# Optimization experiments

Measured on AMD Instinct MI355X. Metric: run time of the kernel, lower is better.

Reference implementation:

```python
import jax, jax.numpy as jnp
import numpy as np

N_NODES = 50000
N_EDGES = 600000
IN_CH = 128
HID_CH = 128
OUT_CH = 16
N_GRAPHS = 512


def gcn_conv(x, edge_index, W, b, n_nodes):
    """PyG GCNConv: add self-loops, symmetric deg normalization, linear, scatter-add."""
    src = edge_index[0]
    dst = edge_index[1]
    loop = jnp.arange(n_nodes, dtype=edge_index.dtype)
    src = jnp.concatenate([src, loop])  # [E+N]
    dst = jnp.concatenate([dst, loop])
    ones = jnp.ones(src.shape[0], dtype=x.dtype)
    deg = jax.ops.segment_sum(ones, dst, num_segments=n_nodes)  # in-degree incl. self-loop
    dinv = jnp.where(deg > 0, jax.lax.rsqrt(deg), 0.0)
    norm = dinv[src] * dinv[dst]  # [E+N]
    h = x @ W  # [N, out] linear-then-propagate, as in PyG GCNConv
    msg = h[src] * norm[:, None]  # gather + scale
    out = jax.ops.segment_sum(msg, dst, num_segments=n_nodes)
    return out + b


def global_mean_pool(x, batch, num_graphs):
    sums = jax.ops.segment_sum(x, batch, num_segments=num_graphs)
    cnt = jax.ops.segment_sum(jnp.ones(x.shape[0], dtype=x.dtype), batch, num_segments=num_graphs)
    return sums / jnp.maximum(cnt, 1.0)[:, None]


def setup_inputs() -> dict:
    key = jax.random.key(0)
    ks = jax.random.split(key, 8)
    x = jax.random.normal(ks[0], (N_NODES, IN_CH), dtype=jnp.float32)
    edge_index = jax.random.randint(ks[1], (2, N_EDGES), 0, N_NODES, dtype=jnp.int64 if jax.config.jax_enable_x64 else jnp.int32)
    batch = jnp.sort(jax.random.randint(ks[2], (N_NODES,), 0, N_GRAPHS, dtype=edge_index.dtype))
    s1 = 1.0 / np.sqrt(IN_CH)
    s2 = 1.0 / np.sqrt(HID_CH)
    W1 = jax.random.uniform(ks[3], (IN_CH, HID_CH), jnp.float32, -s1, s1)
    b1 = jnp.zeros((HID_CH,), jnp.float32)
    W2 = jax.random.uniform(ks[4], (HID_CH, HID_CH), jnp.float32, -s2, s2)
    b2 = jnp.zeros((HID_CH,), jnp.float32)
    Wfc = jax.random.uniform(ks[5], (HID_CH, OUT_CH), jnp.float32, -s2, s2)
    bfc = jax.random.uniform(ks[6], (OUT_CH,), jnp.float32, -s2, s2)
    return {"x": x, "edge_index": edge_index, "batch": batch,
            "W1": W1, "b1": b1, "W2": W2, "b2": b2, "Wfc": Wfc, "bfc": bfc}


def reference(x, edge_index, batch, W1, b1, W2, b2, Wfc, bfc):
    n = x.shape[0]
    h = jax.nn.relu(gcn_conv(x, edge_index, W1, b1, n))
    # dropout is identity in eval mode (training=False)
    h = jax.nn.relu(gcn_conv(h, edge_index, W2, b2, n))
    g = global_mean_pool(h, batch, N_GRAPHS)  # [G, hidden]
    out = jax.nn.sigmoid(g @ Wfc + bfc)  # [G, out]
    return out
```

## Files before the change

kernel.cpp:

```cpp
#include <hip/hip_runtime.h>
#include <hip/hip_fp16.h>
#include <math.h>

#define NN 50000
#define CH 128
#define NG 512
#define OCH 16
#define CAP 64
#define NBINS 196
#define HB 147

typedef _Float16 half8 __attribute__((ext_vector_type(8)));
typedef float f32x4 __attribute__((ext_vector_type(4)));
typedef float f32x2 __attribute__((ext_vector_type(2)));


__device__ __forceinline__ void unpack_fp8x8(unsigned a0, unsigned a1, float* o) {
    f32x2 a = __builtin_amdgcn_cvt_pk_f32_fp8((int)a0, false);
    f32x2 b = __builtin_amdgcn_cvt_pk_f32_fp8((int)a0, true);
    f32x2 c = __builtin_amdgcn_cvt_pk_f32_fp8((int)a1, false);
    f32x2 d = __builtin_amdgcn_cvt_pk_f32_fp8((int)a1, true);
    o[0] = a[0]; o[1] = a[1]; o[2] = b[0]; o[3] = b[1];
    o[4] = c[0]; o[5] = c[1]; o[6] = d[0]; o[7] = d[1];
}

__device__ __forceinline__ void unpack_fp8x16(uint4 v, float* o) {
    unpack_fp8x8(v.x, v.y, o);
    unpack_fp8x8(v.z, v.w, o + 8);
}

__device__ __forceinline__ unsigned char f32_to_fp8(float v) {
    int r = __builtin_amdgcn_cvt_pk_fp8_f32(v, v, 0, false);
    return (unsigned char)(r & 0xFF);
}


__device__ __forceinline__ void gemm1_body(const float* __restrict__ A, const _Float16* __restrict__ Wt,
                                           unsigned char* __restrict__ C, int n, int blk) {
    int wave = threadIdx.x >> 6;
    int lane = threadIdx.x & 63;
    int base = blk * 64 + wave * 16;
    if (base >= n) return;
    int ma = lane & 15;
    int kb = lane >> 4;

    f32x4 acc[8];
#pragma unroll
    for (int t = 0; t < 8; ++t) acc[t] = (f32x4){0.f, 0.f, 0.f, 0.f};

#pragma unroll
    for (int kk = 0; kk < 4; ++kk) {
        int k0 = kk * 32 + kb * 8;
        const float* ap = A + (size_t)(base + ma) * CH + k0;
        float4 a0 = ((const float4*)ap)[0];
        float4 a1 = ((const float4*)ap)[1];
        half8 af;
        af[0] = (_Float16)a0.x; af[1] = (_Float16)a0.y; af[2] = (_Float16)a0.z; af[3] = (_Float16)a0.w;
        af[4] = (_Float16)a1.x; af[5] = (_Float16)a1.y; af[6] = (_Float16)a1.z; af[7] = (_Float16)a1.w;
#pragma unroll
        for (int tn = 0; tn < 8; ++tn) {
            half8 bf = *(const half8*)(Wt + (size_t)(tn * 16 + ma) * CH + k0);
            acc[tn] = __builtin_amdgcn_mfma_f32_16x16x32_f16(af, bf, acc[tn], 0, 0, 0);
        }
    }

    int r0 = base + kb * 4;
#pragma unroll
    for (int tn = 0; tn < 8; ++tn) {
#pragma unroll
        for (int r = 0; r < 4; ++r) {
            C[(size_t)(r0 + r) * CH + tn * 16 + ma] = f32_to_fp8(acc[tn][r]);
        }
    }
}


__global__ __launch_bounds__(256) void k1_hist_init_gemm1_k(const int* __restrict__ dst, int e, int* __restrict__ tableT,
                                                            const int* __restrict__ batch, int n, int* __restrict__ gstart,
                                                            const float* __restrict__ W1, const float* __restrict__ W2,
                                                            _Float16* __restrict__ Wt1, _Float16* __restrict__ Wt2,
                                                            const float* __restrict__ x, unsigned char* __restrict__ h1,
                                                            int* __restrict__ tickets) {
    if ((int)blockIdx.x < HB) {
        __shared__ int hist[NBINS];
        for (int i = threadIdx.x; i < NBINS; i += 256) hist[i] = 0;
        __syncthreads();
#pragma unroll
        for (int j = 0; j < 4; ++j) {
            int idx = blockIdx.x * 4096 + j * 1024 + threadIdx.x * 4;
            if (idx + 3 < e) {
                int4 d = *(const int4*)&dst[idx];
                atomicAdd(&hist[d.x >> 8], 1);
                atomicAdd(&hist[d.y >> 8], 1);
                atomicAdd(&hist[d.z >> 8], 1);
                atomicAdd(&hist[d.w >> 8], 1);
            } else {
                for (int k = idx; k < e && k < idx + 4; ++k) atomicAdd(&hist[dst[k] >> 8], 1);
            }
        }
        __syncthreads();
        for (int i = threadIdx.x; i < NBINS; i += 256) tableT[i * HB + blockIdx.x] = hist[i];
    } else if ((int)blockIdx.x < HB + 66) {
        int i = ((int)blockIdx.x - HB) * 256 + threadIdx.x;
        if (i < 2) tickets[i] = 0;
        if (i <= NG) {
            int lo = 0, hi = n;
            while (lo < hi) {
                int mid = (lo + hi) >> 1;
                if (batch[mid] < i) lo = mid + 1; else hi = mid;
            }
            gstart[i] = lo;
        }
        if (i < CH * CH) {
            int k = i >> 7, c = i & 127;
            Wt1[c * CH + k] = (_Float16)W1[i];
            Wt2[c * CH + k] = (_Float16)W2[i];
        }
    } else {
        gemm1_body(x, Wt1, h1, n, blockIdx.x - (HB + 66));
    }
}


__global__ __launch_bounds__(256) void scanAB_k(int* __restrict__ tableT, int* __restrict__ binsum,
                                                int* __restrict__ bin_start, int* __restrict__ ticket) {
    int w = threadIdx.x >> 6, lane = threadIdx.x & 63;
    int bin = blockIdx.x * 4 + w;
    {
        int* row = tableT + bin * HB;
        int b3 = lane * 3;
        int v0 = (b3     < HB) ? row[b3]     : 0;
        int v1 = (b3 + 1 < HB) ? row[b3 + 1] : 0;
        int v2 = (b3 + 2 < HB) ? row[b3 + 2] : 0;
        int s = v0 + v1 + v2;
        int x = s;
#pragma unroll
        for (int off = 1; off < 64; off <<= 1) {
            int y = __shfl_up(x, off);
            if (lane >= off) x += y;
        }
        int excl = x - s;
        if (b3     < HB) row[b3]     = excl;
        if (b3 + 1 < HB) row[b3 + 1] = excl + v0;
        if (b3 + 2 < HB) row[b3 + 2] = excl + v0 + v1;
        if (lane == 63) binsum[bin] = x;
    }
    __syncthreads();
    __threadfence();
    __shared__ int lastBlk;
    if (threadIdx.x == 0) lastBlk = (atomicAdd(ticket, 1) == (int)gridDim.x - 1) ? 1 : 0;
    __syncthreads();
    if (lastBlk) {
        __threadfence();
        __shared__ int s[256];
        int t = threadIdx.x;
        int v = (t < NBINS) ? binsum[t] : 0;
        s[t] = v;
        __syncthreads();
        for (int off = 1; off < 256; off <<= 1) {
            int u = (t >= off) ? s[t - off] : 0;
            __syncthreads();
            s[t] += u;
            __syncthreads();
        }
        if (t < NBINS) bin_start[t] = s[t] - v;
        if (t == NBINS - 1) bin_start[NBINS] = s[t];
    }
}


__global__ __launch_bounds__(256) void scatter_k(const int* __restrict__ src, const int* __restrict__ dst, int e,
                                                 const int* __restrict__ tableT, const int* __restrict__ bin_start,
                                                 unsigned int* __restrict__ binned) {
    __shared__ int cur[NBINS];
    for (int i = threadIdx.x; i < NBINS; i += 256) cur[i] = bin_start[i] + tableT[i * HB + blockIdx.x];
    __syncthreads();
#pragma unroll
    for (int j = 0; j < 4; ++j) {
        int idx = blockIdx.x * 4096 + j * 1024 + threadIdx.x * 4;
        if (idx + 3 < e) {
            int4 d = *(const int4*)&dst[idx];
            int4 s = *(const int4*)&src[idx];
            int p0 = atomicAdd(&cur[d.x >> 8], 1);
            int p1 = atomicAdd(&cur[d.y >> 8], 1);
            int p2 = atomicAdd(&cur[d.z >> 8], 1);
            int p3 = atomicAdd(&cur[d.w >> 8], 1);
            binned[p0] = (unsigned)s.x | ((unsigned)(d.x & 255) << 16);
            binned[p1] = (unsigned)s.y | ((unsigned)(d.y & 255) << 16);
            binned[p2] = (unsigned)s.z | ((unsigned)(d.z & 255) << 16);
            binned[p3] = (unsigned)s.w | ((unsigned)(d.w & 255) << 16);
        } else {
            for (int k = idx; k < e && k < idx + 4; ++k) {
                int d = dst[k];
                int p = atomicAdd(&cur[d >> 8], 1);
                binned[p] = (unsigned)src[k] | ((unsigned)(d & 255) << 16);
            }
        }
    }
}


__global__ __launch_bounds__(256) void bucket_k(const unsigned int* __restrict__ binned,
                                                const int* __restrict__ bin_start,
                                                int* __restrict__ cursor, int* __restrict__ csr, int n) {
    __shared__ int cur2[256];
    cur2[threadIdx.x] = 0;
    __syncthreads();
    int lo = bin_start[blockIdx.x], hi = bin_start[blockIdx.x + 1];
    for (int i = lo + threadIdx.x; i < hi; i += 256) {
        unsigned int p = binned[i];
        int local = p >> 16;
        int node = ((int)blockIdx.x << 8) | local;
        int pos = atomicAdd(&cur2[local], 1);
        if (pos < CAP) csr[(size_t)node * CAP + pos] = (int)(p & 0xFFFFu);
    }
    __syncthreads();
    int node = blockIdx.x * 256 + threadIdx.x;
    if (node < n) cursor[node] = cur2[threadIdx.x];
}


__global__ __launch_bounds__(256) void agg1_gemm2_k(const unsigned char* __restrict__ h1,
                                                    const int* __restrict__ cursor, const int* __restrict__ csr,
                                                    const float* __restrict__ b1, const _Float16* __restrict__ Wt2,
                                                    unsigned char* __restrict__ h2, int n) {
    __shared__ _Float16 xs[32][136];
    int local = threadIdx.x >> 3;
    int node = blockIdx.x * 32 + local;
    int lane = threadIdx.x & 7;
    const uint4* H = (const uint4*)h1;

    if (node < n) {
        int deg = cursor[node];
        float dv = rsqrtf((float)deg + 1.0f);
        int degc = deg > CAP ? CAP : deg;

        float acc[16];
        {
            float t[16];
            unpack_fp8x16(H[(size_t)node * 8 + lane], t);
#pragma unroll
            for (int j = 0; j < 16; ++j) acc[j] = t[j] * dv;
        }
        const int4* row4 = (const int4*)(csr + (size_t)node * CAP);
        int i = 0;
        for (; i + 4 <= degc; i += 4) {
            int4 s4 = row4[i >> 2];
            uint4 v0 = H[(size_t)s4.x * 8 + lane];
            uint4 v1 = H[(size_t)s4.y * 8 + lane];
            uint4 v2 = H[(size_t)s4.z * 8 + lane];
            uint4 v3 = H[(size_t)s4.w * 8 + lane];
            float w0 = rsqrtf((float)cursor[s4.x] + 1.0f);
            float w1 = rsqrtf((float)cursor[s4.y] + 1.0f);
            float w2 = rsqrtf((float)cursor[s4.z] + 1.0f);
            float w3 = rsqrtf((float)cursor[s4.w] + 1.0f);
            float t0[16], t1[16], t2[16], t3[16];
            unpack_fp8x16(v0, t0); unpack_fp8x16(v1, t1);
            unpack_fp8x16(v2, t2); unpack_fp8x16(v3, t3);
#pragma unroll
            for (int j = 0; j < 16; ++j) {
                acc[j] = fmaf(t0[j], w0, acc[j]);
                acc[j] = fmaf(t1[j], w1, acc[j]);
                acc[j] = fmaf(t2[j], w2, acc[j]);
                acc[j] = fmaf(t3[j], w3, acc[j]);
            }
        }
        for (; i < degc; ++i) {
            int s = csr[(size_t)node * CAP + i];
            float w = rsqrtf((float)cursor[s] + 1.0f);
            float t[16];
            unpack_fp8x16(H[(size_t)s * 8 + lane], t);
#pragma unroll
            for (int j = 0; j < 16; ++j) acc[j] = fmaf(t[j], w, acc[j]);
        }

        half8 hv0, hv1;
#pragma unroll
        for (int q = 0; q < 4; ++q) {
            float4 bb = ((const float4*)b1)[4 * lane + q];
            float r0 = fmaxf(fmaf(acc[4 * q + 0], dv, bb.x), 0.f);
            float r1 = fmaxf(fmaf(acc[4 * q + 1], dv, bb.y), 0.f);
            float r2 = fmaxf(fmaf(acc[4 * q + 2], dv, bb.z), 0.f);
            float r3 = fmaxf(fmaf(acc[4 * q + 3], dv, bb.w), 0.f);
            if (q < 2) {
                hv0[4 * q + 0] = (_Float16)r0; hv0[4 * q + 1] = (_Float16)r1;
                hv0[4 * q + 2] = (_Float16)r2; hv0[4 * q + 3] = (_Float16)r3;
            } else {
                hv1[4 * (q - 2) + 0] = (_Float16)r0; hv1[4 * (q - 2) + 1] = (_Float16)r1;
                hv1[4 * (q - 2) + 2] = (_Float16)r2; hv1[4 * (q - 2) + 3] = (_Float16)r3;
            }
        }
        ((half8*)&xs[local][lane * 16])[0] = hv0;
        ((half8*)&xs[local][lane * 16])[1] = hv1;
    } else {
        half8 z = (half8){0, 0, 0, 0, 0, 0, 0, 0};
        ((half8*)&xs[local][lane * 16])[0] = z;
        ((half8*)&xs[local][lane * 16])[1] = z;
    }
    __syncthreads();

    int wave = threadIdx.x >> 6;
    int l = threadIdx.x & 63;
    int ma = l & 15;
    int kb = l >> 4;
    f32x4 acc00 = (f32x4){0.f, 0.f, 0.f, 0.f}, acc01 = acc00, acc10 = acc00, acc11 = acc00;
#pragma unroll
    for (int kk = 0; kk < 4; ++kk) {
        int k0 = kk * 32 + kb * 8;
        half8 af0 = *(const half8*)&xs[ma][k0];
        half8 af1 = *(const half8*)&xs[16 + ma][k0];
        half8 bf0 = *(const half8*)(Wt2 + (size_t)((wave * 2 + 0) * 16 + ma) * CH + k0);
        half8 bf1 = *(const half8*)(Wt2 + (size_t)((wave * 2 + 1) * 16 + ma) * CH + k0);
        acc00 = __builtin_amdgcn_mfma_f32_16x16x32_f16(af0, bf0, acc00, 0, 0, 0);
        acc01 = __builtin_amdgcn_mfma_f32_16x16x32_f16(af0, bf1, acc01, 0, 0, 0);
        acc10 = __builtin_amdgcn_mfma_f32_16x16x32_f16(af1, bf0, acc10, 0, 0, 0);
        acc11 = __builtin_amdgcn_mfma_f32_16x16x32_f16(af1, bf1, acc11, 0, 0, 0);
    }
    int base = blockIdx.x * 32;
#pragma unroll
    for (int rt = 0; rt < 2; ++rt) {
        int gr0 = base + rt * 16 + kb * 4;
        float dv2[4];
#pragma unroll
        for (int r = 0; r < 4; ++r) dv2[r] = (gr0 + r < n) ? rsqrtf((float)cursor[gr0 + r] + 1.0f) : 0.f;
#pragma unroll
        for (int ct = 0; ct < 2; ++ct) {
            int tn = wave * 2 + ct;
            f32x4 a = (rt == 0) ? (ct == 0 ? acc00 : acc01) : (ct == 0 ? acc10 : acc11);
#pragma unroll
            for (int r = 0; r < 4; ++r) {
                if (gr0 + r < n)
                    h2[(size_t)(gr0 + r) * CH + tn * 16 + ma] = f32_to_fp8(a[r] * dv2[r]);
            }
        }
    }
}


__global__ __launch_bounds__(1024) void agg2_pool_fc_k(const unsigned char* __restrict__ h2,
                                                       const int* __restrict__ cursor, const int* __restrict__ csr,
                                                       const float* __restrict__ b2, const int* __restrict__ gstart,
                                                       const float* __restrict__ Wfc, const float* __restrict__ bfc,
                                                       float* __restrict__ out) {
    __shared__ float psum[128][128];
    __shared__ float psum2[8][128];
    int g = blockIdx.x;
    int group = threadIdx.x >> 3;
    int lane = threadIdx.x & 7;
    int beg = gstart[g], end = gstart[g + 1];
    int c = end - beg;
    const uint4* H = (const uint4*)h2;

    float bias[16];
#pragma unroll
    for (int q = 0; q < 4; ++q) {
        float4 bb = ((const float4*)b2)[4 * lane + q];
        bias[4 * q + 0] = bb.x; bias[4 * q + 1] = bb.y;
        bias[4 * q + 2] = bb.z; bias[4 * q + 3] = bb.w;
    }

    float racc[16];
#pragma unroll
    for (int j = 0; j < 16; ++j) racc[j] = 0.f;

    for (int node = beg + group; node < end; node += 128) {
        int deg = cursor[node];
        float dv = rsqrtf((float)deg + 1.0f);
        int degc = deg > CAP ? CAP : deg;

        float acc[16];
        unpack_fp8x16(H[(size_t)node * 8 + lane], acc);

        const int4* row4 = (const int4*)(csr + (size_t)node * CAP);
        int i = 0;
        for (; i + 4 <= degc; i += 4) {
            int4 s4 = row4[i >> 2];
            uint4 v0 = H[(size_t)s4.x * 8 + lane];
            uint4 v1 = H[(size_t)s4.y * 8 + lane];
            uint4 v2 = H[(size_t)s4.z * 8 + lane];
            uint4 v3 = H[(size_t)s4.w * 8 + lane];
            float t0[16], t1[16], t2[16], t3[16];
            unpack_fp8x16(v0, t0); unpack_fp8x16(v1, t1);
            unpack_fp8x16(v2, t2); unpack_fp8x16(v3, t3);
#pragma unroll
            for (int j = 0; j < 16; ++j) acc[j] += (t0[j] + t1[j]) + (t2[j] + t3[j]);
        }
        for (; i < degc; ++i) {
            int s = csr[(size_t)node * CAP + i];
            float t[16];
            unpack_fp8x16(H[(size_t)s * 8 + lane], t);
#pragma unroll
            for (int j = 0; j < 16; ++j) acc[j] += t[j];
        }

#pragma unroll
        for (int j = 0; j < 16; ++j) racc[j] += fmaxf(fmaf(acc[j], dv, bias[j]), 0.f);
    }

#pragma unroll
    for (int q = 0; q < 4; ++q) {
        float4 v;
        v.x = racc[4 * q + 0]; v.y = racc[4 * q + 1];
        v.z = racc[4 * q + 2]; v.w = racc[4 * q + 3];
        ((float4*)&psum[group][lane * 16])[q] = v;
    }
    __syncthreads();

    {
        int ch = threadIdx.x & 127;
        int seg = threadIdx.x >> 7;
        float s = 0.f;
#pragma unroll
        for (int gg = seg * 16; gg < seg * 16 + 16; ++gg) s += psum[gg][ch];
        psum2[seg][ch] = s;
    }
    __syncthreads();
    int t = threadIdx.x;
    if (t < CH) {
        float s = 0.f;
#pragma unroll
        for (int ss = 0; ss < 8; ++ss) s += psum2[ss][t];
        psum2[0][t] = s / fmaxf((float)c, 1.0f);
    }
    __syncthreads();
    if (t < OCH) {
        float acc = bfc[t];
#pragma unroll 8
        for (int k = 0; k < CH; ++k) acc = fmaf(psum2[0][k], Wfc[k * OCH + t], acc);
        out[(size_t)g * OCH + t] = 1.0f / (1.0f + expf(-acc));
    }
}

extern "C" void kernel_launch(void* const* d_in, const int* in_sizes, int n_in,
                              void* d_out, int out_size, void* d_ws, size_t ws_size,
                              hipStream_t stream) {
    const float* x    = (const float*)d_in[0];
    const int*   edge = (const int*)d_in[1];
    const int*   batch= (const int*)d_in[2];
    const float* W1   = (const float*)d_in[3];
    const float* b1   = (const float*)d_in[4];
    const float* W2   = (const float*)d_in[5];
    const float* b2   = (const float*)d_in[6];
    const float* Wfc  = (const float*)d_in[7];
    const float* bfc  = (const float*)d_in[8];
    float* out = (float*)d_out;

    const int N = NN;
    const int E = in_sizes[1] / 2;
    const int* src = edge;
    const int* dst = edge + E;

    unsigned char* h1 = (unsigned char*)d_ws;
    unsigned char* h2 = h1 + (size_t)N * CH;
    _Float16* Wt1     = (_Float16*)(h2 + (size_t)N * CH);
    _Float16* Wt2     = Wt1 + CH * CH;
    int* cursor       = (int*)(Wt2 + CH * CH);
    int* gstart       = cursor + N;
    int* csr          = gstart + NG + 4;
    int* tableT       = csr + (size_t)N * CAP;
    int* binsum       = tableT + NBINS * HB;
    int* bin_start    = binsum + 256;
    int* tickets      = bin_start + 208;
    unsigned int* binned = (unsigned int*)(tickets + 16);

    const int G = (N + 63) / 64;

    k1_hist_init_gemm1_k<<<HB + 66 + G, 256, 0, stream>>>(dst, E, tableT, batch, N, gstart,
                                                          W1, W2, Wt1, Wt2, x, h1, tickets);
    scanAB_k<<<49, 256, 0, stream>>>(tableT, binsum, bin_start, &tickets[0]);
    scatter_k<<<HB, 256, 0, stream>>>(src, dst, E, tableT, bin_start, binned);
    bucket_k<<<NBINS, 256, 0, stream>>>(binned, bin_start, cursor, csr, N);
    agg1_gemm2_k<<<(N + 31) / 32, 256, 0, stream>>>(h1, cursor, csr, b1, Wt2, h2, N);
    agg2_pool_fc_k<<<NG, 1024, 0, stream>>>(h2, cursor, csr, b2, gstart, Wfc, bfc, out);
}
```

Before: 105.5 us.

## Split layer-2 features into channel halves and precompute fp16 inverse sqrt degrees

The layer-2 hidden features are now stored as two 64-channel halves, and the final aggregation/pool kernel runs twice, once per half. Each pass gathers a smaller working set, which should fit better in cache. The second pass combines both halves for the FC layer. Per-node inverse sqrt degrees are also computed once in the bucketing kernel as fp16, so the layer-1 aggregation loads a 2-byte weight instead of reading the int degree and calling rsqrt per edge. The costs are an extra kernel launch, re-reading the CSR lists twice, and reduced precision in the normalization weights.

New measurement: 103.4 us. 1.02x faster.

```diff
diff --git a/kernel.cpp b/kernel.cpp
--- a/kernel.cpp
+++ b/kernel.cpp
@@ -202,7 +202,8 @@
 
 __global__ __launch_bounds__(256) void bucket_k(const unsigned int* __restrict__ binned,
                                                 const int* __restrict__ bin_start,
-                                                int* __restrict__ cursor, int* __restrict__ csr, int n) {
+                                                int* __restrict__ cursor, int* __restrict__ csr,
+                                                __half* __restrict__ dinv16, int n) {
     __shared__ int cur2[256];
     cur2[threadIdx.x] = 0;
     __syncthreads();
@@ -216,14 +217,20 @@
     }
     __syncthreads();
     int node = blockIdx.x * 256 + threadIdx.x;
-    if (node < n) cursor[node] = cur2[threadIdx.x];
+    if (node < n) {
+        int deg = cur2[threadIdx.x];
+        cursor[node] = deg;
+        dinv16[node] = __float2half(rsqrtf((float)deg + 1.0f));
+    }
 }
 
 
 __global__ __launch_bounds__(256) void agg1_gemm2_k(const unsigned char* __restrict__ h1,
                                                     const int* __restrict__ cursor, const int* __restrict__ csr,
+                                                    const __half* __restrict__ dinv16,
                                                     const float* __restrict__ b1, const _Float16* __restrict__ Wt2,
-                                                    unsigned char* __restrict__ h2, int n) {
+                                                    unsigned char* __restrict__ h2a, unsigned char* __restrict__ h2b,
+                                                    int n) {
     __shared__ _Float16 xs[32][136];
     int local = threadIdx.x >> 3;
     int node = blockIdx.x * 32 + local;
@@ -250,10 +257,10 @@
             uint4 v1 = H[(size_t)s4.y * 8 + lane];
             uint4 v2 = H[(size_t)s4.z * 8 + lane];
             uint4 v3 = H[(size_t)s4.w * 8 + lane];
-            float w0 = rsqrtf((float)cursor[s4.x] + 1.0f);
-            float w1 = rsqrtf((float)cursor[s4.y] + 1.0f);
-            float w2 = rsqrtf((float)cursor[s4.z] + 1.0f);
-            float w3 = rsqrtf((float)cursor[s4.w] + 1.0f);
+            float w0 = __half2float(dinv16[s4.x]);
+            float w1 = __half2float(dinv16[s4.y]);
+            float w2 = __half2float(dinv16[s4.z]);
+            float w3 = __half2float(dinv16[s4.w]);
             float t0[16], t1[16], t2[16], t3[16];
             unpack_fp8x16(v0, t0); unpack_fp8x16(v1, t1);
             unpack_fp8x16(v2, t2); unpack_fp8x16(v3, t3);
@@ -267,7 +274,7 @@
         }
         for (; i < degc; ++i) {
             int s = csr[(size_t)node * CAP + i];
-            float w = rsqrtf((float)cursor[s] + 1.0f);
+            float w = __half2float(dinv16[s]);
             float t[16];
             unpack_fp8x16(H[(size_t)s * 8 + lane], t);
 #pragma unroll
@@ -326,35 +333,40 @@
 #pragma unroll
         for (int ct = 0; ct < 2; ++ct) {
             int tn = wave * 2 + ct;
+            int col = tn * 16 + ma;
+            unsigned char* dstp = (col < 64) ? h2a : h2b;
+            int cidx = col & 63;
             f32x4 a = (rt == 0) ? (ct == 0 ? acc00 : acc01) : (ct == 0 ? acc10 : acc11);
 #pragma unroll
             for (int r = 0; r < 4; ++r) {
                 if (gr0 + r < n)
-                    h2[(size_t)(gr0 + r) * CH + tn * 16 + ma] = f32_to_fp8(a[r] * dv2[r]);
-            }
-        }
-    }
-}
-
-
-__global__ __launch_bounds__(1024) void agg2_pool_fc_k(const unsigned char* __restrict__ h2,
-                                                       const int* __restrict__ cursor, const int* __restrict__ csr,
-                                                       const float* __restrict__ b2, const int* __restrict__ gstart,
-                                                       const float* __restrict__ Wfc, const float* __restrict__ bfc,
-                                                       float* __restrict__ out) {
-    __shared__ float psum[128][128];
-    __shared__ float psum2[8][128];
+                    dstp[(size_t)(gr0 + r) * 64 + cidx] = f32_to_fp8(a[r] * dv2[r]);
+            }
+        }
+    }
+}
+
+
+template <int HALF>
+__global__ __launch_bounds__(512) void agg2_half_k(const unsigned char* __restrict__ h2h,
+                                                   const int* __restrict__ cursor, const int* __restrict__ csr,
+                                                   const float* __restrict__ b2, const int* __restrict__ gstart,
+                                                   float* __restrict__ pooled0,
+                                                   const float* __restrict__ Wfc, const float* __restrict__ bfc,
+                                                   float* __restrict__ out) {
+    __shared__ float psum[128][64];
+    __shared__ float psum2[8][64];
     int g = blockIdx.x;
-    int group = threadIdx.x >> 3;
-    int lane = threadIdx.x & 7;
+    int group = threadIdx.x >> 2;
+    int lane = threadIdx.x & 3;
     int beg = gstart[g], end = gstart[g + 1];
     int c = end - beg;
-    const uint4* H = (const uint4*)h2;
+    const uint4* H = (const uint4*)h2h;
 
     float bias[16];
 #pragma unroll
     for (int q = 0; q < 4; ++q) {
-        float4 bb = ((const float4*)b2)[4 * lane + q];
+        float4 bb = ((const float4*)b2)[HALF * 16 + lane * 4 + q];
         bias[4 * q + 0] = bb.x; bias[4 * q + 1] = bb.y;
         bias[4 * q + 2] = bb.z; bias[4 * q + 3] = bb.w;
     }
@@ -369,16 +381,16 @@
         int degc = deg > CAP ? CAP : deg;
 
         float acc[16];
-        unpack_fp8x16(H[(size_t)node * 8 + lane], acc);
+        unpack_fp8x16(H[(size_t)node * 4 + lane], acc);
 
         const int4* row4 = (const int4*)(csr + (size_t)node * CAP);
         int i = 0;
         for (; i + 4 <= degc; i += 4) {
             int4 s4 = row4[i >> 2];
-            uint4 v0 = H[(size_t)s4.x * 8 + lane];
-            uint4 v1 = H[(size_t)s4.y * 8 + lane];
-            uint4 v2 = H[(size_t)s4.z * 8 + lane];
-            uint4 v3 = H[(size_t)s4.w * 8 + lane];
+            uint4 v0 = H[(size_t)s4.x * 4 + lane];
+            uint4 v1 = H[(size_t)s4.y * 4 + lane];
+            uint4 v2 = H[(size_t)s4.z * 4 + lane];
+            uint4 v3 = H[(size_t)s4.w * 4 + lane];
             float t0[16], t1[16], t2[16], t3[16];
             unpack_fp8x16(v0, t0); unpack_fp8x16(v1, t1);
             unpack_fp8x16(v2, t2); unpack_fp8x16(v3, t3);
@@ -388,7 +400,7 @@
         for (; i < degc; ++i) {
             int s = csr[(size_t)node * CAP + i];
             float t[16];
-            unpack_fp8x16(H[(size_t)s * 8 + lane], t);
+            unpack_fp8x16(H[(size_t)s * 4 + lane], t);
 #pragma unroll
             for (int j = 0; j < 16; ++j) acc[j] += t[j];
         }
@@ -407,8 +419,8 @@
     __syncthreads();
 
     {
-        int ch = threadIdx.x & 127;
-        int seg = threadIdx.x >> 7;
+        int ch = threadIdx.x & 63;
+        int seg = threadIdx.x >> 6;
         float s = 0.f;
 #pragma unroll
         for (int gg = seg * 16; gg < seg * 16 + 16; ++gg) s += psum[gg][ch];
@@ -416,18 +428,25 @@
     }
     __syncthreads();
     int t = threadIdx.x;
-    if (t < CH) {
+    if (t < 64) {
         float s = 0.f;
 #pragma unroll
         for (int ss = 0; ss < 8; ++ss) s += psum2[ss][t];
-        psum2[0][t] = s / fmaxf((float)c, 1.0f);
-    }
-    __syncthreads();
-    if (t < OCH) {
-        float acc = bfc[t];
+        float val = s / fmaxf((float)c, 1.0f);
+        if (HALF == 0) pooled0[(size_t)g * 64 + t] = val;
+        else psum2[0][t] = val;
+    }
+    if (HALF == 1) {
+        __syncthreads();
+        if (t < OCH) {
+            float acc = bfc[t];
+            const float* p0 = pooled0 + (size_t)g * 64;
 #pragma unroll 8
-        for (int k = 0; k < CH; ++k) acc = fmaf(psum2[0][k], Wfc[k * OCH + t], acc);
-        out[(size_t)g * OCH + t] = 1.0f / (1.0f + expf(-acc));
+            for (int k = 0; k < 64; ++k) acc = fmaf(p0[k], Wfc[k * OCH + t], acc);
+#pragma unroll 8
+            for (int k = 0; k < 64; ++k) acc = fmaf(psum2[0][k], Wfc[(64 + k) * OCH + t], acc);
+            out[(size_t)g * OCH + t] = 1.0f / (1.0f + expf(-acc));
+        }
     }
 }
 
@@ -450,17 +469,20 @@
     const int* src = edge;
     const int* dst = edge + E;
 
-    unsigned char* h1 = (unsigned char*)d_ws;
-    unsigned char* h2 = h1 + (size_t)N * CH;
-    _Float16* Wt1     = (_Float16*)(h2 + (size_t)N * CH);
-    _Float16* Wt2     = Wt1 + CH * CH;
-    int* cursor       = (int*)(Wt2 + CH * CH);
-    int* gstart       = cursor + N;
-    int* csr          = gstart + NG + 4;
-    int* tableT       = csr + (size_t)N * CAP;
-    int* binsum       = tableT + NBINS * HB;
-    int* bin_start    = binsum + 256;
-    int* tickets      = bin_start + 208;
+    unsigned char* h1  = (unsigned char*)d_ws;
+    unsigned char* h2a = h1 + (size_t)N * CH;
+    unsigned char* h2b = h2a + (size_t)N * 64;
+    _Float16* Wt1      = (_Float16*)(h2b + (size_t)N * 64);
+    _Float16* Wt2      = Wt1 + CH * CH;
+    __half* dinv16     = (__half*)(Wt2 + CH * CH);
+    float* pooled0     = (float*)(dinv16 + N);
+    int* cursor        = (int*)(pooled0 + (size_t)NG * 64);
+    int* gstart        = cursor + N;
+    int* csr           = gstart + NG + 8;
+    int* tableT        = csr + (size_t)N * CAP;
+    int* binsum        = tableT + NBINS * HB;
+    int* bin_start     = binsum + 256;
+    int* tickets       = bin_start + 208;
     unsigned int* binned = (unsigned int*)(tickets + 16);
 
     const int G = (N + 63) / 64;
@@ -469,7 +491,8 @@
                                                           W1, W2, Wt1, Wt2, x, h1, tickets);
     scanAB_k<<<49, 256, 0, stream>>>(tableT, binsum, bin_start, &tickets[0]);
     scatter_k<<<HB, 256, 0, stream>>>(src, dst, E, tableT, bin_start, binned);
-    bucket_k<<<NBINS, 256, 0, stream>>>(binned, bin_start, cursor, csr, N);
-    agg1_gemm2_k<<<(N + 31) / 32, 256, 0, stream>>>(h1, cursor, csr, b1, Wt2, h2, N);
-    agg2_pool_fc_k<<<NG, 1024, 0, stream>>>(h2, cursor, csr, b2, gstart, Wfc, bfc, out);
-}
+    bucket_k<<<NBINS, 256, 0, stream>>>(binned, bin_start, cursor, csr, dinv16, N);
+    agg1_gemm2_k<<<(N + 31) / 32, 256, 0, stream>>>(h1, cursor, csr, dinv16, b1, Wt2, h2a, h2b, N);
+    agg2_half_k<0><<<NG, 512, 0, stream>>>(h2a, cursor, csr, b2, gstart, pooled0, Wfc, bfc, out);
+    agg2_half_k<1><<<NG, 512, 0, stream>>>(h2b, cursor, csr, b2, gstart, pooled0, Wfc, bfc, out);
+}
```
